# Kernel tuning notes

Measured on AMD Instinct MI355X. Metric: run time of the kernel, lower is better.

Reference implementation:

```python
import jax, jax.numpy as jnp
import numpy as np
from jax import lax


def ternarize(w):
    # TWN-style ternarization: threshold delta = 0.7*mean|w|, scale alpha =
    # mean |w| over surviving entries; straight-through in backward.
    aw = jnp.abs(w)
    delta = 0.7 * jnp.mean(aw)
    mask = (aw > delta).astype(w.dtype)
    alpha = jnp.sum(aw * mask) / jnp.maximum(jnp.sum(mask), 1.0)
    q = alpha * jnp.sign(w) * mask
    return w + lax.stop_gradient(q - w)


def conv2d(x, w, b):
    # x: [N,C,H,W], w: [O,I,kh,kw]
    y = lax.conv_general_dilated(x, w, window_strides=(1, 1), padding='VALID',
                                 dimension_numbers=('NCHW', 'OIHW', 'NCHW'))
    return y + b[None, :, None, None]


def maxpool2(x):
    return lax.reduce_window(x, -jnp.inf, lax.max,
                             window_dimensions=(1, 1, 2, 2),
                             window_strides=(1, 1, 2, 2), padding='VALID')


def setup_inputs() -> dict:
    key = jax.random.key(0)
    ks = jax.random.split(key, 11)
    n_classes = 10
    x = jax.random.normal(ks[0], (1024, 1, 32, 32), dtype=jnp.float32)
    # Kaiming-ish scaled params
    w1 = jax.random.normal(ks[1], (32, 1, 5, 5), jnp.float32) * (1.0 / np.sqrt(1 * 25))
    b1 = jnp.zeros((32,), jnp.float32)
    w2 = jax.random.normal(ks[2], (64, 32, 5, 5), jnp.float32) * (1.0 / np.sqrt(32 * 25))
    b2 = jnp.zeros((64,), jnp.float32)
    w3 = jax.random.normal(ks[3], (120, 64, 5, 5), jnp.float32) * (1.0 / np.sqrt(64 * 25))
    b3 = jnp.zeros((120,), jnp.float32)
    fw1 = jax.random.normal(ks[4], (84, 120), jnp.float32) * (1.0 / np.sqrt(120))
    fb1 = jnp.zeros((84,), jnp.float32)
    fw2 = jax.random.normal(ks[5], (n_classes, 84), jnp.float32) * (1.0 / np.sqrt(84))
    fb2 = jnp.zeros((n_classes,), jnp.float32)
    return {"x": x, "w1": w1, "b1": b1, "w2": w2, "b2": b2,
            "w3": w3, "b3": b3, "fw1": fw1, "fb1": fb1, "fw2": fw2, "fb2": fb2}


def reference(x, w1, b1, w2, b2, w3, b3, fw1, fb1, fw2, fb2):
    h = jnp.tanh(conv2d(x, ternarize(w1), b1))   # [N,32,28,28]
    h = maxpool2(h)                              # [N,32,14,14]
    h = jnp.tanh(conv2d(h, ternarize(w2), b2))   # [N,64,10,10]
    h = maxpool2(h)                              # [N,64,5,5]
    h = jnp.tanh(conv2d(h, ternarize(w3), b3))   # [N,120,1,1]
    h = h.reshape(h.shape[0], -1)                # [N,120]
    h = jnp.tanh(h @ ternarize(fw1).T + fb1)     # [N,84]
    logits = h @ ternarize(fw2).T + fb2          # [N,n_classes]
    probs = jax.nn.softmax(logits, axis=1)
    return (logits, probs)
```

## Files before the change

### kernel.cpp

```cpp
#include <hip/hip_runtime.h>
#include <hip/hip_bf16.h>
#include <math.h>


typedef __attribute__((ext_vector_type(8))) short bf16x8;
typedef __attribute__((ext_vector_type(4))) float f32x4;

static const size_t OFF_PB    = 0;
static const size_t OFF_W1B   = 256;
static const size_t OFF_W2B   = 1056;
static const size_t OFF_W3B   = 26656;
static const size_t OFF_FW1T  = 129056;
static const size_t OFF_FW2T  = 139136;
static const size_t OFF_P2B   = 139976;

#define BPT 16

__device__ __forceinline__ ushort f2bf(float v) {
    unsigned u = __float_as_uint(v);
    unsigned r = (u + 0x7FFFu + ((u >> 16) & 1u)) >> 16;
    return (ushort)r;
}
__device__ __forceinline__ float bf2f(ushort h) {
    return __uint_as_float((unsigned)h << 16);
}

__device__ __forceinline__ float tanh_fast(float x) {
    float e = __expf(-2.0f * fabsf(x));
    float r = 1.0f - 2.0f * e / (1.0f + e);
    return copysignf(r, x);
}

__device__ __forceinline__ void tensor_select(int tensor,
        const float* w1, const float* w2, const float* w3,
        const float* fw1, const float* fw2,
        const float*& src, int& O, int& K) {
    switch (tensor) {
        case 0: src = w1;  O = 32;  K = 25;   break;
        case 1: src = w2;  O = 64;  K = 800;  break;
        case 2: src = w3;  O = 120; K = 1600; break;
        case 3: src = fw1; O = 84;  K = 120;  break;
        default: src = fw2; O = 10; K = 84;   break;
    }
}

__device__ __forceinline__ float block_sum_256(float v, float* sbuf) {
    #pragma unroll
    for (int off = 32; off > 0; off >>= 1) v += __shfl_down(v, off);
    const int wid = threadIdx.x >> 6;
    if ((threadIdx.x & 63) == 0) sbuf[wid] = v;
    __syncthreads();
    return sbuf[0] + sbuf[1] + sbuf[2] + sbuf[3];
}

__device__ __forceinline__ float alpha_of(const float* pb, int tensor) {
    float s1 = 0.f, c = 0.f;
    #pragma unroll
    for (int i = 0; i < BPT; ++i) {
        s1 += pb[80 + tensor * BPT + i];
        c  += pb[160 + tensor * BPT + i];
    }
    return s1 / fmaxf(c, 1.0f);
}

__global__ __launch_bounds__(256)
void tern_pass1(const float* w1, const float* w2, const float* w3,
                const float* fw1, const float* fw2, float* pb) {
    __shared__ float sbuf[4];
    const int tensor = blockIdx.x / BPT;
    const int blk    = blockIdx.x % BPT;
    const float* src; int O, K;
    tensor_select(tensor, w1, w2, w3, fw1, fw2, src, O, K);
    const int n = O * K;
    float s = 0.f;
    for (int i = blk * 256 + threadIdx.x; i < n; i += BPT * 256)
        s += fabsf(src[i]);
    s = block_sum_256(s, sbuf);
    if (threadIdx.x == 0) pb[tensor * BPT + blk] = s;
}

__global__ __launch_bounds__(256)
void tern_pass2(const float* w1, const float* w2, const float* w3,
                const float* fw1, const float* fw2,
                ushort* w1b, ushort* w2b, ushort* w3b,
                float* fw1t, float* fw2t, float* pb) {
    __shared__ float sbuf[4];
    const int tensor = blockIdx.x / BPT;
    const int blk    = blockIdx.x % BPT;
    const float* src; int O, K;
    tensor_select(tensor, w1, w2, w3, fw1, fw2, src, O, K);
    const int n = O * K;
    float tot = 0.f;
    #pragma unroll
    for (int i = 0; i < BPT; ++i) tot += pb[tensor * BPT + i];
    const float delta = 0.7f * tot / (float)n;

    const ushort BP = 0x3F80u, BN = 0xBF80u;
    float s1 = 0.f, cnt = 0.f;

    if (tensor == 0) {
        for (int j = blk * 256 + threadIdx.x; j < 1024; j += BPT * 256) {
            const int oc = j >> 5, kk = j & 31;
            ushort qb = 0;
            if (kk < 25) {
                float w = src[oc * 25 + kk];
                float aw = fabsf(w);
                if (aw > delta) { s1 += aw; cnt += 1.f; qb = (w > 0.f) ? BP : BN; }
            }
            w1b[j] = qb;
        }
    } else if (tensor == 2) {
        for (int i = blk * 256 + threadIdx.x; i < 128 * 1600; i += BPT * 256) {
            ushort qb = 0;
            if (i < n) {
                float w = src[i];
                float aw = fabsf(w);
                if (aw > delta) { s1 += aw; cnt += 1.f; qb = (w > 0.f) ? BP : BN; }
            }
            w3b[i] = qb;
        }
    } else if (tensor == 1) {
        for (int i = blk * 256 + threadIdx.x; i < n; i += BPT * 256) {
            float w = src[i];
            float aw = fabsf(w);
            ushort qb = 0;
            if (aw > delta) { s1 += aw; cnt += 1.f; qb = (w > 0.f) ? BP : BN; }
            int oc = i / 800;
            int r  = i - oc * 800;
            int ic = r / 25;
            int tap = r - ic * 25;
            w2b[oc * 800 + tap * 32 + ic] = qb;
        }
    } else {
        float* dst = (tensor == 3) ? fw1t : fw2t;
        for (int i = blk * 256 + threadIdx.x; i < n; i += BPT * 256) {
            float w = src[i];
            float aw = fabsf(w);
            float q = 0.f;
            if (aw > delta) { s1 += aw; cnt += 1.f; q = (w > 0.f) ? 1.f : -1.f; }
            int o = i / K;
            int k = i - o * K;
            dst[k * O + o] = q;
        }
    }
    s1 = block_sum_256(s1, sbuf);
    __syncthreads();
    cnt = block_sum_256(cnt, sbuf);
    if (threadIdx.x == 0) {
        pb[80 + tensor * BPT + blk]  = s1;
        pb[160 + tensor * BPT + blk] = cnt;
    }
}

#define C2PF 4
__device__ __forceinline__ void conv2_all(
        const ushort* __restrict__ w2b, const ushort* sxt,
        int n0, int mt0, int lane, f32x4 acc[4][2]) {
    const int col = lane & 15, quad = lane >> 4;
    const ushort* abase[4];
    #pragma unroll
    for (int mi = 0; mi < 4; ++mi) {
        int m = (mt0 + mi) * 16 + col;
        m = m < 100 ? m : 99;
        const int oh = m / 10, ow = m - oh * 10;
        abase[mi] = sxt + (oh * 14 + ow) * 40 + quad * 8;
    }
    const ushort* wb0 = w2b + (size_t)(n0 + col) * 800 + quad * 8;
    const ushort* wb1 = wb0 + 16 * 800;
    bf16x8 pb0[C2PF], pb1[C2PF];
    #pragma unroll
    for (int i = 0; i < C2PF; ++i) {
        pb0[i] = *(const bf16x8*)(wb0 + i * 32);
        pb1[i] = *(const bf16x8*)(wb1 + i * 32);
    }
    #pragma unroll
    for (int tap = 0; tap < 25; ++tap) {
        const int slot = tap & (C2PF - 1);
        const bf16x8 b0 = pb0[slot];
        const bf16x8 b1 = pb1[slot];
        if (tap + C2PF < 25) {
            pb0[slot] = *(const bf16x8*)(wb0 + (tap + C2PF) * 32);
            pb1[slot] = *(const bf16x8*)(wb1 + (tap + C2PF) * 32);
        }
        const int kh = tap / 5, kw = tap - kh * 5;
        const int aoff = (kh * 14 + kw) * 40;
        #pragma unroll
        for (int mi = 0; mi < 4; ++mi) {
            bf16x8 af = *(const bf16x8*)(abase[mi] + aoff);
            acc[mi][0] = __builtin_amdgcn_mfma_f32_16x16x32_bf16(af, b0, acc[mi][0], 0, 0, 0);
            acc[mi][1] = __builtin_amdgcn_mfma_f32_16x16x32_bf16(af, b1, acc[mi][1], 0, 0, 0);
        }
    }
}

__global__ __launch_bounds__(256, 4)
void conv12_kernel(const float* __restrict__ x, const ushort* __restrict__ w1b,
                   const float* __restrict__ b1, const ushort* __restrict__ w2b,
                   const float* __restrict__ b2, const float* __restrict__ pb,
                   ushort* __restrict__ p2b) {
    __shared__ __align__(16) char smem[37328];
    ushort* A      = (ushort*)smem;
    float*  hb2    = (float*) smem;
    ushort* sxt    = (ushort*)(smem + 19584);
    ushort* sxb    = (ushort*)(smem + 35264);
    float*  salpha = (float*) (smem + 37312);

    const int n = blockIdx.x;
    const int t = threadIdx.x;
    const int wave = t >> 6, lane = t & 63;
    const int col = lane & 15, quad = lane >> 4;

    bf16x8 B0 = *(const bf16x8*)(w1b + col * 32 + quad * 8);
    bf16x8 B1 = *(const bf16x8*)(w1b + (col + 16) * 32 + quad * 8);
    const float b1a = b1[col];
    const float b1b = b1[col + 16];

    {
        float4 v = ((const float4*)(x + (size_t)n * 1024))[t];
        ushort4 q;
        q.x = f2bf(v.x); q.y = f2bf(v.y); q.z = f2bf(v.z); q.w = f2bf(v.w);
        *(ushort4*)(sxb + t * 4) = q;
        if (t == 0) salpha[0] = alpha_of(pb, 0);
        if (t == 1) salpha[1] = alpha_of(pb, 1);
    }
    __syncthreads();

    const float a1 = salpha[0];
    for (int c = 0; c < 3; ++c) {
        const int tbase = (c == 0) ? 0 : (17 + 16 * (c - 1));
        const int ct    = (c == 0) ? 17 : 16;
        const int pbase = tbase * 16;
        const int rows  = ct * 16;

        for (int r = t; r < rows; r += 256) {
            const int p   = pbase + r;
            const int pb4 = p >> 2, sub = p & 3;
            const int oh = 2 * (pb4 / 14) + (sub >> 1);
            const int ow = 2 * (pb4 % 14) + (sub & 1);
            ushort v[25];
            #pragma unroll
            for (int kh = 0; kh < 5; ++kh) {
                const ushort* rr = sxb + (oh + kh) * 32 + ow;
                v[kh*5+0]=rr[0]; v[kh*5+1]=rr[1]; v[kh*5+2]=rr[2];
                v[kh*5+3]=rr[3]; v[kh*5+4]=rr[4];
            }
            uint2* arow = (uint2*)(A + r * 36);
            #pragma unroll
            for (int j = 0; j < 6; ++j) {
                uint2 w;
                w.x = (unsigned)v[4*j]   | ((unsigned)v[4*j+1] << 16);
                w.y = (unsigned)v[4*j+2] | ((unsigned)v[4*j+3] << 16);
                arow[j] = w;
            }
            uint2 w6; w6.x = (unsigned)v[24]; w6.y = 0u;
            arow[6] = w6;
            uint2 w7; w7.x = 0u; w7.y = 0u;
            arow[7] = w7;
        }
        __syncthreads();

        for (int tl = wave; tl < ct; tl += 4) {
            const ushort* ap = A + (tl * 16 + col) * 36 + quad * 8;
            ushort4 lo = *(const ushort4*)ap;
            ushort4 hi = *(const ushort4*)(ap + 4);
            bf16x8 af;
            af[0]=(short)lo.x; af[1]=(short)lo.y; af[2]=(short)lo.z; af[3]=(short)lo.w;
            af[4]=(short)hi.x; af[5]=(short)hi.y; af[6]=(short)hi.z; af[7]=(short)hi.w;
            f32x4 z = {};
            f32x4 c0 = __builtin_amdgcn_mfma_f32_16x16x32_bf16(af, B0, z, 0, 0, 0);
            f32x4 c1 = __builtin_amdgcn_mfma_f32_16x16x32_bf16(af, B1, z, 0, 0, 0);
            const int pos2 = (pbase >> 2) + tl * 4 + quad;
            const float h01 = bf2f(f2bf(fmaxf(c0[0], c0[1])));
            const float h23 = bf2f(f2bf(fmaxf(c0[2], c0[3])));
            sxt[pos2 * 40 + col] =
                f2bf(tanh_fast(fmaf(a1, fmaxf(h01, h23), b1a)));
            const float g01 = bf2f(f2bf(fmaxf(c1[0], c1[1])));
            const float g23 = bf2f(f2bf(fmaxf(c1[2], c1[3])));
            sxt[pos2 * 40 + col + 16] =
                f2bf(tanh_fast(fmaf(a1, fmaxf(g01, g23), b1b)));
        }
        __syncthreads();
    }

    const int n0  = (wave & 1) * 32;
    const int mt0 = (wave >> 1) * 4;
    f32x4 acc2[4][2] = {};
    conv2_all(w2b, sxt, n0, mt0, lane, acc2);

    {
        #pragma unroll
        for (int mi = 0; mi < 4; ++mi) {
            const int mrow = (mt0 + mi) * 16 + quad * 4;
            if (mrow < 100) {
                #pragma unroll
                for (int np = 0; np < 2; ++np) {
                    const int oc = n0 + np * 16 + col;
                    float2 hm;
                    hm.x = fmaxf(acc2[mi][np][0], acc2[mi][np][1]);
                    hm.y = fmaxf(acc2[mi][np][2], acc2[mi][np][3]);
                    *(float2*)(&hb2[oc * 50 + (mrow >> 1)]) = hm;
                }
            }
        }
    }
    __syncthreads();

    const float a2 = salpha[1];
    for (int idx = t; idx < 1600; idx += 256) {
        const int oc = idx / 25, r = idx - oc * 25;
        const int ph = r / 5, pw = r - ph * 5;
        const float* hb = &hb2[oc * 50 + ph * 10 + pw];
        float m = fmaxf(hb[0], hb[5]);
        p2b[(size_t)n * 1600 + idx] = f2bf(tanh_fast(fmaf(a2, m, b2[oc])));
    }
}

__global__ __launch_bounds__(256)
void conv3fc_kernel(const ushort* __restrict__ p2b, const ushort* __restrict__ w3b,
                    const float* __restrict__ b3, const float* __restrict__ pb,
                    const float* __restrict__ fw1t, const float* __restrict__ fb1,
                    const float* __restrict__ fw2t, const float* __restrict__ fb2,
                    float* __restrict__ out) {
    __shared__ __align__(16) char redmem[32768];
    __shared__ __align__(16) float h3s[16][120];
    __shared__ __align__(16) float fw1s[120 * 84];
    __shared__ __align__(16) float fw2s[84 * 10];
    __shared__ float salpha[3];
    float (*red)[64][8][4] = (float (*)[64][8][4])redmem;
    float* sh4 = (float*)redmem;
    float* sl  = (float*)(redmem + 16 * 84 * 4);

    const int t = threadIdx.x;
    const int wave = t >> 6, lane = t & 63;
    const int col = lane & 15, quad = lane >> 4;
    const int img0 = blockIdx.x * 16;

    for (int i = t; i < 2520; i += 256)
        ((float4*)fw1s)[i] = ((const float4*)fw1t)[i];
    if (t < 210) ((float4*)fw2s)[t] = ((const float4*)fw2t)[t];
    if (t == 0) salpha[0] = alpha_of(pb, 2);
    if (t == 1) salpha[1] = alpha_of(pb, 3);
    if (t == 2) salpha[2] = alpha_of(pb, 4);

    const int kstart = (wave < 2) ? wave * 13 : 26 + (wave - 2) * 12;
    const int steps  = (wave < 2) ? 13 : 12;
    const ushort* Abase = p2b + (size_t)(img0 + col) * 1600 + kstart * 32 + quad * 8;
    const ushort* Bbase = w3b + (size_t)col * 1600 + kstart * 32 + quad * 8;

    f32x4 acc[8] = {};
    for (int s = 0; s < steps; ++s) {
        const bf16x8 af = *(const bf16x8*)(Abase + s * 32);
        #pragma unroll
        for (int nt = 0; nt < 8; ++nt) {
            const bf16x8 bf = *(const bf16x8*)(Bbase + (size_t)nt * 16 * 1600 + s * 32);
            acc[nt] = __builtin_amdgcn_mfma_f32_16x16x32_bf16(af, bf, acc[nt], 0, 0, 0);
        }
    }
    #pragma unroll
    for (int nt = 0; nt < 8; ++nt)
        #pragma unroll
        for (int r = 0; r < 4; ++r) red[wave][lane][nt][r] = acc[nt][r];
    __syncthreads();

    {
        const float a3 = salpha[0];
        const int l = t & 63, vh = t >> 6;
        const int lcol = l & 15, lquad = l >> 4;
        const int img = lquad * 4 + vh;
        #pragma unroll
        for (int nt = 0; nt < 8; ++nt) {
            const int oc = nt * 16 + lcol;
            if (oc < 120) {
                float s = red[0][l][nt][vh] + red[1][l][nt][vh]
                        + red[2][l][nt][vh] + red[3][l][nt][vh];
                h3s[img][oc] = tanh_fast(fmaf(a3, s, b3[oc]));
            }
        }
    }
    __syncthreads();

    {
        const float af1 = salpha[1];
        for (int task = t; task < 1344; task += 256) {
            const int img = task / 84, oc = task - img * 84;
            float a = 0.f;
            #pragma unroll 4
            for (int k = 0; k < 120; ++k)
                a = fmaf(fw1s[k * 84 + oc], h3s[img][k], a);
            sh4[img * 84 + oc] = tanh_fast(fmaf(af1, a, fb1[oc]));
        }
    }
    __syncthreads();

    if (t < 160) {
        const float af2 = salpha[2];
        const int img = t / 10, oc = t - img * 10;
        float a2 = 0.f;
        #pragma unroll 4
        for (int k = 0; k < 84; ++k)
            a2 = fmaf(fw2s[k * 10 + oc], sh4[img * 84 + k], a2);
        const float lg = fmaf(af2, a2, fb2[oc]);
        sl[img * 10 + oc] = lg;
        out[(size_t)(img0 + img) * 10 + oc] = lg;
    }
    __syncthreads();

    if (t < 160) {
        const int img = t / 10, oc = t - img * 10;
        float m = -INFINITY;
        #pragma unroll
        for (int i = 0; i < 10; ++i) m = fmaxf(m, sl[img * 10 + i]);
        float s = 0.f;
        #pragma unroll
        for (int i = 0; i < 10; ++i) s += expf(sl[img * 10 + i] - m);
        out[10240 + (size_t)(img0 + img) * 10 + oc] = expf(sl[img * 10 + oc] - m) / s;
    }
}

extern "C" void kernel_launch(void* const* d_in, const int* in_sizes, int n_in,
                              void* d_out, int out_size, void* d_ws, size_t ws_size,
                              hipStream_t stream) {
    const float* x   = (const float*)d_in[0];
    const float* w1  = (const float*)d_in[1];
    const float* b1  = (const float*)d_in[2];
    const float* w2  = (const float*)d_in[3];
    const float* b2  = (const float*)d_in[4];
    const float* w3  = (const float*)d_in[5];
    const float* b3  = (const float*)d_in[6];
    const float* fw1 = (const float*)d_in[7];
    const float* fb1 = (const float*)d_in[8];
    const float* fw2 = (const float*)d_in[9];
    const float* fb2 = (const float*)d_in[10];

    float* ws = (float*)d_ws;
    float*  pb   = ws + OFF_PB;
    ushort* w1b  = (ushort*)(ws + OFF_W1B);
    ushort* w2b  = (ushort*)(ws + OFF_W2B);
    ushort* w3b  = (ushort*)(ws + OFF_W3B);
    float*  fw1t = ws + OFF_FW1T;
    float*  fw2t = ws + OFF_FW2T;
    ushort* p2b  = (ushort*)(ws + OFF_P2B);
    float*  out  = (float*)d_out;

    tern_pass1<<<5 * BPT, 256, 0, stream>>>(w1, w2, w3, fw1, fw2, pb);
    tern_pass2<<<5 * BPT, 256, 0, stream>>>(w1, w2, w3, fw1, fw2,
                                            w1b, w2b, w3b, fw1t, fw2t, pb);
    conv12_kernel<<<1024, 256, 0, stream>>>(x, w1b, b1, w2b, b2, pb, p2b);
    conv3fc_kernel<<<64, 256, 0, stream>>>(p2b, w3b, b3, pb,
                                           fw1t, fb1, fw2t, fb2, out);
}
```

Baseline: 160.3 us.

## Split conv3 output tiles across 16 waves in conv3fc kernel

The conv3+FC kernel now launches 1024 threads per block instead of 256. The 16 waves cover a 4-way K split times a 4-way output-tile split, so each wave computes 2 MFMA output tiles instead of 8. The shared reduction buffer is changed to a lane-contiguous layout for cheaper shared-memory access, and the epilogue loops are re-strided for the larger block. The aim is more parallelism in a kernel with only 64 blocks; in exchange, the A fragment is loaded redundantly by four waves and the larger blocks cap registers per thread.

```diff
diff --git a/kernel.cpp b/kernel.cpp
--- a/kernel.cpp
+++ b/kernel.cpp
@@ -315,7 +315,7 @@
     }
 }
 
-__global__ __launch_bounds__(256)
+__global__ __launch_bounds__(1024)
 void conv3fc_kernel(const ushort* __restrict__ p2b, const ushort* __restrict__ w3b,
                     const float* __restrict__ b3, const float* __restrict__ pb,
                     const float* __restrict__ fw1t, const float* __restrict__ fb1,
@@ -326,7 +326,7 @@
     __shared__ __align__(16) float fw1s[120 * 84];
     __shared__ __align__(16) float fw2s[84 * 10];
     __shared__ float salpha[3];
-    float (*red)[64][8][4] = (float (*)[64][8][4])redmem;
+    float (*red)[8][4][64] = (float (*)[8][4][64])redmem;
     float* sh4 = (float*)redmem;
     float* sl  = (float*)(redmem + 16 * 84 * 4);
 
@@ -334,45 +334,54 @@
     const int wave = t >> 6, lane = t & 63;
     const int col = lane & 15, quad = lane >> 4;
     const int img0 = blockIdx.x * 16;
-
-    for (int i = t; i < 2520; i += 256)
+    const int kg  = wave & 3;
+    const int ntg = wave >> 2;
+
+    for (int i = t; i < 2520; i += 1024)
         ((float4*)fw1s)[i] = ((const float4*)fw1t)[i];
     if (t < 210) ((float4*)fw2s)[t] = ((const float4*)fw2t)[t];
     if (t == 0) salpha[0] = alpha_of(pb, 2);
     if (t == 1) salpha[1] = alpha_of(pb, 3);
     if (t == 2) salpha[2] = alpha_of(pb, 4);
 
-    const int kstart = (wave < 2) ? wave * 13 : 26 + (wave - 2) * 12;
-    const int steps  = (wave < 2) ? 13 : 12;
+    const int kstart = (kg < 2) ? kg * 13 : 26 + (kg - 2) * 12;
+    const int steps  = (kg < 2) ? 13 : 12;
     const ushort* Abase = p2b + (size_t)(img0 + col) * 1600 + kstart * 32 + quad * 8;
-    const ushort* Bbase = w3b + (size_t)col * 1600 + kstart * 32 + quad * 8;
-
-    f32x4 acc[8] = {};
-    for (int s = 0; s < steps; ++s) {
-        const bf16x8 af = *(const bf16x8*)(Abase + s * 32);
-        #pragma unroll
-        for (int nt = 0; nt < 8; ++nt) {
-            const bf16x8 bf = *(const bf16x8*)(Bbase + (size_t)nt * 16 * 1600 + s * 32);
-            acc[nt] = __builtin_amdgcn_mfma_f32_16x16x32_bf16(af, bf, acc[nt], 0, 0, 0);
-        }
-    }
-    #pragma unroll
-    for (int nt = 0; nt < 8; ++nt)
-        #pragma unroll
-        for (int r = 0; r < 4; ++r) red[wave][lane][nt][r] = acc[nt][r];
+
+    f32x4 acc[2] = {};
+    {
+        const int nt0 = ntg * 2;
+        const ushort* Bb0 = w3b + (size_t)(nt0 * 16 + col) * 1600 + kstart * 32 + quad * 8;
+        const ushort* Bb1 = Bb0 + (size_t)16 * 1600;
+        for (int s = 0; s < steps; ++s) {
+            const bf16x8 af = *(const bf16x8*)(Abase + s * 32);
+            const bf16x8 b0 = *(const bf16x8*)(Bb0 + s * 32);
+            const bf16x8 b1 = *(const bf16x8*)(Bb1 + s * 32);
+            acc[0] = __builtin_amdgcn_mfma_f32_16x16x32_bf16(af, b0, acc[0], 0, 0, 0);
+            acc[1] = __builtin_amdgcn_mfma_f32_16x16x32_bf16(af, b1, acc[1], 0, 0, 0);
+        }
+        #pragma unroll
+        for (int j = 0; j < 2; ++j)
+            #pragma unroll
+            for (int r = 0; r < 4; ++r)
+                red[kg][nt0 + j][r][lane] = acc[j][r];
+    }
     __syncthreads();
 
     {
         const float a3 = salpha[0];
-        const int l = t & 63, vh = t >> 6;
-        const int lcol = l & 15, lquad = l >> 4;
-        const int img = lquad * 4 + vh;
-        #pragma unroll
-        for (int nt = 0; nt < 8; ++nt) {
-            const int oc = nt * 16 + lcol;
+        #pragma unroll
+        for (int half = 0; half < 2; ++half) {
+            const int idx = t + half * 1024;
+            const int nt  = idx >> 8;
+            const int rem = idx & 255;
+            const int vh  = rem >> 6;
+            const int l   = rem & 63;
+            const int img = ((l >> 4) << 2) + vh;
+            const int oc  = (nt << 4) + (l & 15);
             if (oc < 120) {
-                float s = red[0][l][nt][vh] + red[1][l][nt][vh]
-                        + red[2][l][nt][vh] + red[3][l][nt][vh];
+                float s = red[0][nt][vh][l] + red[1][nt][vh][l]
+                        + red[2][nt][vh][l] + red[3][nt][vh][l];
                 h3s[img][oc] = tanh_fast(fmaf(a3, s, b3[oc]));
             }
         }
@@ -381,7 +390,7 @@
 
     {
         const float af1 = salpha[1];
-        for (int task = t; task < 1344; task += 256) {
+        for (int task = t; task < 1344; task += 1024) {
             const int img = task / 84, oc = task - img * 84;
             float a = 0.f;
             #pragma unroll 4
@@ -446,6 +455,6 @@
     tern_pass2<<<5 * BPT, 256, 0, stream>>>(w1, w2, w3, fw1, fw2,
                                             w1b, w2b, w3b, fw1t, fw2t, pb);
     conv12_kernel<<<1024, 256, 0, stream>>>(x, w1b, b1, w2b, b2, pb, p2b);
-    conv3fc_kernel<<<64, 256, 0, stream>>>(p2b, w3b, b3, pb,
-                                           fw1t, fb1, fw2t, fb2, out);
-}
+    conv3fc_kernel<<<64, 1024, 0, stream>>>(p2b, w3b, b3, pb,
+                                            fw1t, fb1, fw2t, fb2, out);
+}
```

New measurement: 153.0 us. -4.6%, faster.
